# Performance work log

Hardware: AMD Instinct MI355X
Metric: run time of the kernel (lower is better)

Reference implementation:

```python
import jax, jax.numpy as jnp
import numpy as np

EPS = 1e-6
GAMMA = 1.0
NB_EXPERTS = 16
DEPTH = 4  # log2(NB_EXPERTS), complete binary tree
K = 4
ENTROPY_REG = 0.01


def smooth_step(t, gamma=GAMMA):
    # DSelect-k / COMET smooth-step: 0 below -gamma/2, 1 above gamma/2, cubic between
    poly = (-2.0 / gamma ** 3) * t ** 3 + (3.0 / (2.0 * gamma)) * t + 0.5
    return jnp.where(t <= -gamma / 2, 0.0, jnp.where(t >= gamma / 2, 1.0, poly))


def setup_inputs() -> dict:
    key = jax.random.key(0)
    k0, k1, k2, k3 = jax.random.split(key, 4)
    B, D_IN, D_OUT = 8192, 1024, 768
    # h: expert outputs, already stacked (torch code concatenates a list on dim 2)
    h = jax.random.normal(k0, (B, D_OUT, NB_EXPERTS), jnp.float32)
    x = jax.random.normal(k1, (B, D_IN), jnp.float32)
    # selector weights: uniform(-gamma/100, gamma/100), level-order over internal nodes
    sel_w = jax.random.uniform(k2, (NB_EXPERTS - 1, K, D_IN), jnp.float32, -GAMMA / 100, GAMMA / 100)
    # leaf output layers: uniform(-0.05, 0.05) weights, zero bias
    leaf_w = jax.random.uniform(k3, (NB_EXPERTS, K, D_IN), jnp.float32, -0.05, 0.05)
    leaf_b = jnp.zeros((NB_EXPERTS, K), jnp.float32)
    return {"h": h, "x": x, "sel_w": sel_w, "leaf_w": leaf_w, "leaf_b": leaf_b}


def reference(h, x, sel_w, leaf_w, leaf_b):
    B = x.shape[0]
    # gate activations at all internal nodes (level order): (B, E-1, K)
    gates = smooth_step(jnp.einsum('bd,nkd->bnk', x, sel_w))
    # expand root->leaf path products level by level; [left, right] interleave
    # matches the recursive concat order on dim 2 in the torch code
    probs = jnp.ones((B, 1, K), x.dtype)
    start = 0
    for d in range(DEPTH):
        n = 2 ** d
        g = gates[:, start:start + n, :]               # (B, n, K)
        probs = jnp.stack([probs * g, probs * (1.0 - g)], axis=2).reshape(B, 2 * n, K)
        start += n
    # probs: (B, E, K) leaf routing probabilities
    # leaf logits a_bij + log(prob)
    a = jnp.einsum('bd,ekd->bek', x, leaf_w) + leaf_b  # (B, E, K)
    logp = jnp.where(probs < 1e-5, -jnp.inf, jnp.log(probs + 1e-6))
    s = a + logp                                       # (B, E, K)
    # softmax over all k*E leaf slots (flatten order irrelevant to the sums below)
    w = jax.nn.softmax(s.reshape(B, -1), axis=-1).reshape(B, NB_EXPERTS, K)
    # permutation_mask is k stacked identities -> einsum is identity; sum over k
    w_expert = jnp.sum(w, axis=2)                      # (B, E)
    w_norm = w_expert / jnp.sum(w_expert, axis=-1, keepdims=True)
    # aggregate expert outputs
    y_agg = jnp.einsum('bde,be->bd', h, w_norm)        # (B, D_OUT)
    # sparsity statistics (keep torch shapes: w_permuted is (B,1,1,E))
    w4 = w_norm[:, None, None, :]
    s_concat = jnp.where(w4 < 1e-5, jnp.ones_like(w4), jnp.zeros_like(w4))
    soft_averages = jnp.mean(w4, axis=(0, 1, 2))       # (E,)
    hard_averages = jnp.mean(1.0 - s_concat, axis=(0, 1, 2))  # (E,)
    # entropy regularization, summed over leaves = sum over (E,K) per sample
    p = jnp.clip(probs, EPS, None)
    reg = ENTROPY_REG * jnp.mean(jnp.sum(-(p + EPS) * jnp.log(p + EPS), axis=(1, 2)))
    return (y_agg, soft_averages, hard_averages, s_concat, reg)
```

## Files before the change

kernel.cpp:

```cpp
#include <hip/hip_runtime.h>
#include <math.h>

#define NB 8192
#define DIN 1024
#define DOUT 768
#define NE 16

#define BM 128
#define BN 128
#define BK 32
#define KSPLIT 4
#define KCHUNK (DIN / KSPLIT)
#define NTILES (KCHUNK / BK)
#define LDT 36

#define NSEL 60
#define NCOL 124

#define Y_OFF    0
#define SOFT_OFF 6291456
#define HARD_OFF 6291472
#define SC_OFF   6291488
#define REG_OFF  6422560

__device__ __forceinline__ float smooth_step_f(float t) {
  float p = -2.0f * t * t * t + 1.5f * t + 0.5f;
  p = (t <= -0.5f) ? 0.0f : p;
  p = (t >= 0.5f) ? 1.0f : p;
  return p;
}

__global__ __launch_bounds__(256) void k1_gemm(
    const float* __restrict__ x, const float* __restrict__ sel_w,
    const float* __restrict__ leaf_w, float* __restrict__ Gp)
{
  __shared__ float xs[BM * LDT];
  __shared__ float wsm[BN * LDT];
  const int t  = threadIdx.x;
  const int b0 = blockIdx.x * BM;
  const int k0 = blockIdx.y * KCHUNK;
  const int rg = t >> 4;
  const int cg = t & 15;

  float acc[8][8];
#pragma unroll
  for (int i = 0; i < 8; ++i)
#pragma unroll
    for (int j = 0; j < 8; ++j) acc[i][j] = 0.0f;

  int fr[4], fk[4];
#pragma unroll
  for (int m = 0; m < 4; ++m) { int f = t + 256 * m; fr[m] = f >> 3; fk[m] = (f & 7) * 4; }

  float4 px[4], pw[4];
#pragma unroll
  for (int m = 0; m < 4; ++m) {
    int kb = k0 + fk[m];
    px[m] = *(const float4*)(x + (size_t)(b0 + fr[m]) * DIN + kb);
    int c = fr[m];
    if (c < NSEL)      pw[m] = *(const float4*)(sel_w + (size_t)c * DIN + kb);
    else if (c < NCOL) pw[m] = *(const float4*)(leaf_w + (size_t)(c - NSEL) * DIN + kb);
    else               pw[m] = make_float4(0.f, 0.f, 0.f, 0.f);
  }

  for (int kt = 0; kt < NTILES; ++kt) {
#pragma unroll
    for (int m = 0; m < 4; ++m) {
      *(float4*)(&xs[fr[m] * LDT + fk[m]])  = px[m];
      *(float4*)(&wsm[fr[m] * LDT + fk[m]]) = pw[m];
    }
    __syncthreads();
    if (kt + 1 < NTILES) {
      int kb0 = k0 + (kt + 1) * BK;
#pragma unroll
      for (int m = 0; m < 4; ++m) {
        int kb = kb0 + fk[m];
        px[m] = *(const float4*)(x + (size_t)(b0 + fr[m]) * DIN + kb);
        int c = fr[m];
        if (c < NSEL)      pw[m] = *(const float4*)(sel_w + (size_t)c * DIN + kb);
        else if (c < NCOL) pw[m] = *(const float4*)(leaf_w + (size_t)(c - NSEL) * DIN + kb);
        else               pw[m] = make_float4(0.f, 0.f, 0.f, 0.f);
      }
    }
#pragma unroll 4
    for (int kk = 0; kk < BK; ++kk) {
      float xv[8], wv[8];
#pragma unroll
      for (int i = 0; i < 8; ++i) xv[i] = xs[(rg + 16 * i) * LDT + kk];
#pragma unroll
      for (int j = 0; j < 8; ++j) wv[j] = wsm[(cg + 16 * j) * LDT + kk];
#pragma unroll
      for (int i = 0; i < 8; ++i)
#pragma unroll
        for (int j = 0; j < 8; ++j)
          acc[i][j] = fmaf(xv[i], wv[j], acc[i][j]);
    }
    __syncthreads();
  }

  const int ks = blockIdx.y;
#pragma unroll
  for (int i = 0; i < 8; ++i) {
    int gr = b0 + rg + 16 * i;
#pragma unroll
    for (int j = 0; j < 8; ++j) {
      int c = cg + 16 * j;
      Gp[((size_t)ks * NB + gr) * BN + c] = acc[i][j];
    }
  }
}

__global__ __launch_bounds__(256) void k2_rows(
    const float* __restrict__ Gp, const float* __restrict__ leaf_b,
    float* __restrict__ wnorm, float* __restrict__ out)
{
  const int b = blockIdx.x * 256 + threadIdx.x;
  const size_t rb = (size_t)b * BN;

  float s_arr[64];
  float rsum = 0.0f;

#pragma unroll
  for (int k = 0; k < 4; ++k) {
    float gt[15];
#pragma unroll
    for (int n = 0; n < 15; ++n) {
      float v = 0.0f;
#pragma unroll
      for (int s = 0; s < KSPLIT; ++s) v += Gp[(size_t)s * NB * BN + rb + n * 4 + k];
      gt[n] = smooth_step_f(v);
    }
#pragma unroll
    for (int l = 0; l < 16; ++l) {
      float g0 = gt[0];
      float g1 = gt[1 + (l >> 3)];
      float g2 = gt[3 + (l >> 2)];
      float g3 = gt[7 + (l >> 1)];
      float f0 = ((l >> 3) & 1) ? (1.0f - g0) : g0;
      float f1 = ((l >> 2) & 1) ? (1.0f - g1) : g1;
      float f2 = ((l >> 1) & 1) ? (1.0f - g2) : g2;
      float f3 = (l & 1)        ? (1.0f - g3) : g3;
      float p = ((f0 * f1) * f2) * f3;
      float pc = fmaxf(p, 1e-6f);
      float lg = logf(pc + 1e-6f);
      rsum += -(pc + 1e-6f) * lg;
      float av = 0.0f;
#pragma unroll
      for (int s = 0; s < KSPLIT; ++s) av += Gp[(size_t)s * NB * BN + rb + NSEL + l * 4 + k];
      av += leaf_b[l * 4 + k];
      s_arr[l * 4 + k] = (p < 1e-5f) ? -INFINITY : (av + lg);
    }
  }

  float m = s_arr[0];
#pragma unroll
  for (int i = 1; i < 64; ++i) m = fmaxf(m, s_arr[i]);

  float we[16];
#pragma unroll
  for (int e = 0; e < 16; ++e) we[e] = 0.0f;
  float sum = 0.0f;
#pragma unroll
  for (int e = 0; e < 16; ++e)
#pragma unroll
    for (int k = 0; k < 4; ++k) {
      float wv = expf(s_arr[e * 4 + k] - m);
      sum += wv;
      we[e] += wv;
    }
  float inv = 1.0f / sum;

  float softp[16], hardp[16];
#pragma unroll
  for (int e = 0; e < 16; ++e) {
    float wn = we[e] * inv;
    softp[e] = wn;
    float sc = (wn < 1e-5f) ? 1.0f : 0.0f;
    hardp[e] = 1.0f - sc;
    wnorm[(size_t)b * NE + e] = wn;
    out[SC_OFF + (size_t)b * NE + e] = sc;
  }

#pragma unroll
  for (int e = 0; e < 16; ++e) {
    float v = softp[e];
    v += __shfl_down(v, 32, 64); v += __shfl_down(v, 16, 64); v += __shfl_down(v, 8, 64);
    v += __shfl_down(v, 4, 64);  v += __shfl_down(v, 2, 64);  v += __shfl_down(v, 1, 64);
    if ((threadIdx.x & 63) == 0) atomicAdd(&out[SOFT_OFF + e], v * (1.0f / (float)NB));
    float hv = hardp[e];
    hv += __shfl_down(hv, 32, 64); hv += __shfl_down(hv, 16, 64); hv += __shfl_down(hv, 8, 64);
    hv += __shfl_down(hv, 4, 64);  hv += __shfl_down(hv, 2, 64);  hv += __shfl_down(hv, 1, 64);
    if ((threadIdx.x & 63) == 0) atomicAdd(&out[HARD_OFF + e], hv * (1.0f / (float)NB));
  }
  {
    float v = rsum;
    v += __shfl_down(v, 32, 64); v += __shfl_down(v, 16, 64); v += __shfl_down(v, 8, 64);
    v += __shfl_down(v, 4, 64);  v += __shfl_down(v, 2, 64);  v += __shfl_down(v, 1, 64);
    if ((threadIdx.x & 63) == 0) atomicAdd(&out[REG_OFF], v * (0.01f / (float)NB));
  }
}

__global__ __launch_bounds__(256) void k3_yagg(
    const float* __restrict__ h, const float* __restrict__ wnorm,
    float* __restrict__ out)
{
  const int b = blockIdx.x;
  __shared__ float wl[NE];
  if (threadIdx.x < NE) wl[threadIdx.x] = wnorm[(size_t)b * NE + threadIdx.x];
  __syncthreads();
  float w[NE];
#pragma unroll
  for (int e = 0; e < NE; ++e) w[e] = wl[e];

#pragma unroll
  for (int mm = 0; mm < 3; ++mm) {
    int d = threadIdx.x + 256 * mm;
    const float4* hp = (const float4*)(h + ((size_t)b * DOUT + d) * NE);
    float4 h0 = hp[0], h1 = hp[1], h2 = hp[2], h3 = hp[3];
    float acc;
    acc  = h0.x * w[0]  + h0.y * w[1]  + h0.z * w[2]  + h0.w * w[3];
    acc += h1.x * w[4]  + h1.y * w[5]  + h1.z * w[6]  + h1.w * w[7];
    acc += h2.x * w[8]  + h2.y * w[9]  + h2.z * w[10] + h2.w * w[11];
    acc += h3.x * w[12] + h3.y * w[13] + h3.z * w[14] + h3.w * w[15];
    out[(size_t)b * DOUT + d] = acc;
  }
}

extern "C" void kernel_launch(void* const* d_in, const int* in_sizes, int n_in,
                              void* d_out, int out_size, void* d_ws, size_t ws_size,
                              hipStream_t stream)
{
  const float* h      = (const float*)d_in[0];
  const float* x      = (const float*)d_in[1];
  const float* sel_w  = (const float*)d_in[2];
  const float* leaf_w = (const float*)d_in[3];
  const float* leaf_b = (const float*)d_in[4];
  float* out = (float*)d_out;

  float* wnorm = (float*)d_ws;
  float* Gp    = wnorm + (size_t)NB * NE;

  hipMemsetAsync(out + SOFT_OFF, 0, 32 * sizeof(float), stream);
  hipMemsetAsync(out + REG_OFF, 0, sizeof(float), stream);

  k1_gemm<<<dim3(NB / BM, KSPLIT), 256, 0, stream>>>(x, sel_w, leaf_w, Gp);
  k2_rows<<<NB / 256, 256, 0, stream>>>(Gp, leaf_b, wnorm, out);
  k3_yagg<<<NB, 256, 0, stream>>>(h, wnorm, out);
}
```

Measured before the change: 651.8 us.

## Fuse gate GEMM with per-row routing softmax, drop split-K partials

Merges the split-K GEMM kernel and the per-row routing kernel into one kernel. Each block computes a 32-row by 128-column tile over the full K dimension, stages the results in shared memory, and lets 32 threads run the gating, softmax and statistics. This removes the global round trip of four partial-sum buffers and one kernel launch. In exchange it reloads the full weight matrix for every 32 rows and leaves 224 of 256 threads idle during the serial per-row phase.

```diff
diff --git a/kernel.cpp b/kernel.cpp
--- a/kernel.cpp
+++ b/kernel.cpp
@@ -6,18 +6,14 @@
 #define DOUT 768
 #define NE 16
 
-#define BM 128
-#define BN 128
-#define BK 32
-#define KSPLIT 4
-#define KCHUNK (DIN / KSPLIT)
-#define NTILES (KCHUNK / BK)
-#define LDT 36
-
+#define RB 32
+#define KT 64
+#define NT (DIN / KT)
+#define LDW 68
+#define LDG 129
 #define NSEL 60
 #define NCOL 124
 
-#define Y_OFF    0
 #define SOFT_OFF 6291456
 #define HARD_OFF 6291472
 #define SC_OFF   6291488
@@ -30,173 +26,168 @@
   return p;
 }
 
-__global__ __launch_bounds__(256) void k1_gemm(
+__global__ __launch_bounds__(256) void k12_gate(
     const float* __restrict__ x, const float* __restrict__ sel_w,
-    const float* __restrict__ leaf_w, float* __restrict__ Gp)
-{
-  __shared__ float xs[BM * LDT];
-  __shared__ float wsm[BN * LDT];
-  const int t  = threadIdx.x;
-  const int b0 = blockIdx.x * BM;
-  const int k0 = blockIdx.y * KCHUNK;
-  const int rg = t >> 4;
-  const int cg = t & 15;
-
-  float acc[8][8];
-#pragma unroll
-  for (int i = 0; i < 8; ++i)
-#pragma unroll
-    for (int j = 0; j < 8; ++j) acc[i][j] = 0.0f;
-
-  int fr[4], fk[4];
-#pragma unroll
-  for (int m = 0; m < 4; ++m) { int f = t + 256 * m; fr[m] = f >> 3; fk[m] = (f & 7) * 4; }
-
-  float4 px[4], pw[4];
-#pragma unroll
-  for (int m = 0; m < 4; ++m) {
-    int kb = k0 + fk[m];
-    px[m] = *(const float4*)(x + (size_t)(b0 + fr[m]) * DIN + kb);
-    int c = fr[m];
-    if (c < NSEL)      pw[m] = *(const float4*)(sel_w + (size_t)c * DIN + kb);
-    else if (c < NCOL) pw[m] = *(const float4*)(leaf_w + (size_t)(c - NSEL) * DIN + kb);
-    else               pw[m] = make_float4(0.f, 0.f, 0.f, 0.f);
-  }
-
-  for (int kt = 0; kt < NTILES; ++kt) {
-#pragma unroll
-    for (int m = 0; m < 4; ++m) {
-      *(float4*)(&xs[fr[m] * LDT + fk[m]])  = px[m];
-      *(float4*)(&wsm[fr[m] * LDT + fk[m]]) = pw[m];
-    }
-    __syncthreads();
-    if (kt + 1 < NTILES) {
-      int kb0 = k0 + (kt + 1) * BK;
-#pragma unroll
-      for (int m = 0; m < 4; ++m) {
-        int kb = kb0 + fk[m];
-        px[m] = *(const float4*)(x + (size_t)(b0 + fr[m]) * DIN + kb);
-        int c = fr[m];
-        if (c < NSEL)      pw[m] = *(const float4*)(sel_w + (size_t)c * DIN + kb);
-        else if (c < NCOL) pw[m] = *(const float4*)(leaf_w + (size_t)(c - NSEL) * DIN + kb);
-        else               pw[m] = make_float4(0.f, 0.f, 0.f, 0.f);
-      }
-    }
-#pragma unroll 4
-    for (int kk = 0; kk < BK; ++kk) {
-      float xv[8], wv[8];
-#pragma unroll
-      for (int i = 0; i < 8; ++i) xv[i] = xs[(rg + 16 * i) * LDT + kk];
-#pragma unroll
-      for (int j = 0; j < 8; ++j) wv[j] = wsm[(cg + 16 * j) * LDT + kk];
-#pragma unroll
-      for (int i = 0; i < 8; ++i)
-#pragma unroll
-        for (int j = 0; j < 8; ++j)
-          acc[i][j] = fmaf(xv[i], wv[j], acc[i][j]);
-    }
-    __syncthreads();
-  }
-
-  const int ks = blockIdx.y;
-#pragma unroll
-  for (int i = 0; i < 8; ++i) {
-    int gr = b0 + rg + 16 * i;
-#pragma unroll
-    for (int j = 0; j < 8; ++j) {
-      int c = cg + 16 * j;
-      Gp[((size_t)ks * NB + gr) * BN + c] = acc[i][j];
-    }
-  }
-}
-
-__global__ __launch_bounds__(256) void k2_rows(
-    const float* __restrict__ Gp, const float* __restrict__ leaf_b,
+    const float* __restrict__ leaf_w, const float* __restrict__ leaf_b,
     float* __restrict__ wnorm, float* __restrict__ out)
 {
-  const int b = blockIdx.x * 256 + threadIdx.x;
-  const size_t rb = (size_t)b * BN;
-
-  float s_arr[64];
-  float rsum = 0.0f;
-
-#pragma unroll
-  for (int k = 0; k < 4; ++k) {
-    float gt[15];
-#pragma unroll
-    for (int n = 0; n < 15; ++n) {
-      float v = 0.0f;
-#pragma unroll
-      for (int s = 0; s < KSPLIT; ++s) v += Gp[(size_t)s * NB * BN + rb + n * 4 + k];
-      gt[n] = smooth_step_f(v);
-    }
-#pragma unroll
-    for (int l = 0; l < 16; ++l) {
-      float g0 = gt[0];
-      float g1 = gt[1 + (l >> 3)];
-      float g2 = gt[3 + (l >> 2)];
-      float g3 = gt[7 + (l >> 1)];
-      float f0 = ((l >> 3) & 1) ? (1.0f - g0) : g0;
-      float f1 = ((l >> 2) & 1) ? (1.0f - g1) : g1;
-      float f2 = ((l >> 1) & 1) ? (1.0f - g2) : g2;
-      float f3 = (l & 1)        ? (1.0f - g3) : g3;
-      float p = ((f0 * f1) * f2) * f3;
-      float pc = fmaxf(p, 1e-6f);
-      float lg = logf(pc + 1e-6f);
-      rsum += -(pc + 1e-6f) * lg;
-      float av = 0.0f;
-#pragma unroll
-      for (int s = 0; s < KSPLIT; ++s) av += Gp[(size_t)s * NB * BN + rb + NSEL + l * 4 + k];
-      av += leaf_b[l * 4 + k];
-      s_arr[l * 4 + k] = (p < 1e-5f) ? -INFINITY : (av + lg);
-    }
-  }
-
-  float m = s_arr[0];
-#pragma unroll
-  for (int i = 1; i < 64; ++i) m = fmaxf(m, s_arr[i]);
-
-  float we[16];
-#pragma unroll
-  for (int e = 0; e < 16; ++e) we[e] = 0.0f;
-  float sum = 0.0f;
-#pragma unroll
-  for (int e = 0; e < 16; ++e)
+  __shared__ float xs[RB * LDW];
+  __shared__ float wsm[128 * LDW];
+  __shared__ float gsm[RB * LDG];
+  const int t  = threadIdx.x;
+  const int b0 = blockIdx.x * RB;
+  const int tr = t >> 5;
+  const int tc = t & 31;
+
+  float acc[4][4];
+#pragma unroll
+  for (int i = 0; i < 4; ++i)
+#pragma unroll
+    for (int j = 0; j < 4; ++j) acc[i][j] = 0.0f;
+
+  int xr[2], xk[2];
+#pragma unroll
+  for (int m = 0; m < 2; ++m) { int f = t + 256 * m; xr[m] = f >> 4; xk[m] = (f & 15) * 4; }
+  int wc[8], wk[8];
+#pragma unroll
+  for (int m = 0; m < 8; ++m) { int f = t + 256 * m; wc[m] = f >> 4; wk[m] = (f & 15) * 4; }
+
+  float4 px[2], pw[8];
+#pragma unroll
+  for (int m = 0; m < 2; ++m)
+    px[m] = *(const float4*)(x + (size_t)(b0 + xr[m]) * DIN + xk[m]);
+#pragma unroll
+  for (int m = 0; m < 8; ++m) {
+    int c = wc[m];
+    if (c < NSEL)      pw[m] = *(const float4*)(sel_w + (size_t)c * DIN + wk[m]);
+    else if (c < NCOL) pw[m] = *(const float4*)(leaf_w + (size_t)(c - NSEL) * DIN + wk[m]);
+    else               pw[m] = make_float4(0.f, 0.f, 0.f, 0.f);
+  }
+
+  for (int kt = 0; kt < NT; ++kt) {
+#pragma unroll
+    for (int m = 0; m < 2; ++m) *(float4*)(&xs[xr[m] * LDW + xk[m]]) = px[m];
+#pragma unroll
+    for (int m = 0; m < 8; ++m) *(float4*)(&wsm[wc[m] * LDW + wk[m]]) = pw[m];
+    __syncthreads();
+    if (kt + 1 < NT) {
+      int kb = (kt + 1) * KT;
+#pragma unroll
+      for (int m = 0; m < 2; ++m)
+        px[m] = *(const float4*)(x + (size_t)(b0 + xr[m]) * DIN + kb + xk[m]);
+#pragma unroll
+      for (int m = 0; m < 8; ++m) {
+        int c = wc[m];
+        if (c < NSEL)      pw[m] = *(const float4*)(sel_w + (size_t)c * DIN + kb + wk[m]);
+        else if (c < NCOL) pw[m] = *(const float4*)(leaf_w + (size_t)(c - NSEL) * DIN + kb + wk[m]);
+        else               pw[m] = make_float4(0.f, 0.f, 0.f, 0.f);
+      }
+    }
+#pragma unroll 8
+    for (int kk = 0; kk < KT; kk += 4) {
+      float4 xv[4], wv[4];
+#pragma unroll
+      for (int i = 0; i < 4; ++i) xv[i] = *(const float4*)(&xs[(tr + 8 * i) * LDW + kk]);
+#pragma unroll
+      for (int j = 0; j < 4; ++j) wv[j] = *(const float4*)(&wsm[(tc + 32 * j) * LDW + kk]);
+#pragma unroll
+      for (int i = 0; i < 4; ++i)
+#pragma unroll
+        for (int j = 0; j < 4; ++j) {
+          acc[i][j] = fmaf(xv[i].x, wv[j].x, acc[i][j]);
+          acc[i][j] = fmaf(xv[i].y, wv[j].y, acc[i][j]);
+          acc[i][j] = fmaf(xv[i].z, wv[j].z, acc[i][j]);
+          acc[i][j] = fmaf(xv[i].w, wv[j].w, acc[i][j]);
+        }
+    }
+    __syncthreads();
+  }
+
+#pragma unroll
+  for (int i = 0; i < 4; ++i)
+#pragma unroll
+    for (int j = 0; j < 4; ++j)
+      gsm[(tr + 8 * i) * LDG + tc + 32 * j] = acc[i][j];
+  __syncthreads();
+
+  if (t < RB) {
+    const int b = b0 + t;
+    const float* gr = &gsm[t * LDG];
+
+    float s_arr[64];
+    float rsum = 0.0f;
 #pragma unroll
     for (int k = 0; k < 4; ++k) {
-      float wv = expf(s_arr[e * 4 + k] - m);
-      sum += wv;
-      we[e] += wv;
-    }
-  float inv = 1.0f / sum;
-
-  float softp[16], hardp[16];
-#pragma unroll
-  for (int e = 0; e < 16; ++e) {
-    float wn = we[e] * inv;
-    softp[e] = wn;
-    float sc = (wn < 1e-5f) ? 1.0f : 0.0f;
-    hardp[e] = 1.0f - sc;
-    wnorm[(size_t)b * NE + e] = wn;
-    out[SC_OFF + (size_t)b * NE + e] = sc;
-  }
-
-#pragma unroll
-  for (int e = 0; e < 16; ++e) {
-    float v = softp[e];
-    v += __shfl_down(v, 32, 64); v += __shfl_down(v, 16, 64); v += __shfl_down(v, 8, 64);
-    v += __shfl_down(v, 4, 64);  v += __shfl_down(v, 2, 64);  v += __shfl_down(v, 1, 64);
-    if ((threadIdx.x & 63) == 0) atomicAdd(&out[SOFT_OFF + e], v * (1.0f / (float)NB));
-    float hv = hardp[e];
-    hv += __shfl_down(hv, 32, 64); hv += __shfl_down(hv, 16, 64); hv += __shfl_down(hv, 8, 64);
-    hv += __shfl_down(hv, 4, 64);  hv += __shfl_down(hv, 2, 64);  hv += __shfl_down(hv, 1, 64);
-    if ((threadIdx.x & 63) == 0) atomicAdd(&out[HARD_OFF + e], hv * (1.0f / (float)NB));
-  }
-  {
-    float v = rsum;
-    v += __shfl_down(v, 32, 64); v += __shfl_down(v, 16, 64); v += __shfl_down(v, 8, 64);
-    v += __shfl_down(v, 4, 64);  v += __shfl_down(v, 2, 64);  v += __shfl_down(v, 1, 64);
-    if ((threadIdx.x & 63) == 0) atomicAdd(&out[REG_OFF], v * (0.01f / (float)NB));
+      float gt[15];
+#pragma unroll
+      for (int n = 0; n < 15; ++n) gt[n] = smooth_step_f(gr[n * 4 + k]);
+#pragma unroll
+      for (int l = 0; l < 16; ++l) {
+        float g0 = gt[0];
+        float g1 = gt[1 + (l >> 3)];
+        float g2 = gt[3 + (l >> 2)];
+        float g3 = gt[7 + (l >> 1)];
+        float f0 = ((l >> 3) & 1) ? (1.0f - g0) : g0;
+        float f1 = ((l >> 2) & 1) ? (1.0f - g1) : g1;
+        float f2 = ((l >> 1) & 1) ? (1.0f - g2) : g2;
+        float f3 = (l & 1)        ? (1.0f - g3) : g3;
+        float p = ((f0 * f1) * f2) * f3;
+        float pc = fmaxf(p, 1e-6f);
+        float lg = logf(pc + 1e-6f);
+        rsum += -(pc + 1e-6f) * lg;
+        float av = gr[NSEL + l * 4 + k] + leaf_b[l * 4 + k];
+        s_arr[l * 4 + k] = (p < 1e-5f) ? -INFINITY : (av + lg);
+      }
+    }
+
+    float m = s_arr[0];
+#pragma unroll
+    for (int i = 1; i < 64; ++i) m = fmaxf(m, s_arr[i]);
+
+    float we[16];
+#pragma unroll
+    for (int e = 0; e < 16; ++e) we[e] = 0.0f;
+    float sum = 0.0f;
+#pragma unroll
+    for (int e = 0; e < 16; ++e)
+#pragma unroll
+      for (int k = 0; k < 4; ++k) {
+        float wv = expf(s_arr[e * 4 + k] - m);
+        sum += wv;
+        we[e] += wv;
+      }
+    float inv = 1.0f / sum;
+
+    float softp[16], hardp[16];
+#pragma unroll
+    for (int e = 0; e < 16; ++e) {
+      float wn = we[e] * inv;
+      softp[e] = wn;
+      float sc = (wn < 1e-5f) ? 1.0f : 0.0f;
+      hardp[e] = 1.0f - sc;
+      wnorm[(size_t)b * NE + e] = wn;
+      out[SC_OFF + (size_t)b * NE + e] = sc;
+    }
+
+#pragma unroll
+    for (int e = 0; e < 16; ++e) {
+      float v = softp[e];
+      v += __shfl_down(v, 16, 64); v += __shfl_down(v, 8, 64);
+      v += __shfl_down(v, 4, 64);  v += __shfl_down(v, 2, 64); v += __shfl_down(v, 1, 64);
+      float hv = hardp[e];
+      hv += __shfl_down(hv, 16, 64); hv += __shfl_down(hv, 8, 64);
+      hv += __shfl_down(hv, 4, 64);  hv += __shfl_down(hv, 2, 64); hv += __shfl_down(hv, 1, 64);
+      if (t == 0) {
+        atomicAdd(&out[SOFT_OFF + e], v * (1.0f / (float)NB));
+        atomicAdd(&out[HARD_OFF + e], hv * (1.0f / (float)NB));
+      }
+    }
+    {
+      float v = rsum;
+      v += __shfl_down(v, 16, 64); v += __shfl_down(v, 8, 64);
+      v += __shfl_down(v, 4, 64);  v += __shfl_down(v, 2, 64); v += __shfl_down(v, 1, 64);
+      if (t == 0) atomicAdd(&out[REG_OFF], v * (0.01f / (float)NB));
+    }
   }
 }
 
@@ -238,12 +229,10 @@
   float* out = (float*)d_out;
 
   float* wnorm = (float*)d_ws;
-  float* Gp    = wnorm + (size_t)NB * NE;
 
   hipMemsetAsync(out + SOFT_OFF, 0, 32 * sizeof(float), stream);
   hipMemsetAsync(out + REG_OFF, 0, sizeof(float), stream);
 
-  k1_gemm<<<dim3(NB / BM, KSPLIT), 256, 0, stream>>>(x, sel_w, leaf_w, Gp);
-  k2_rows<<<NB / 256, 256, 0, stream>>>(Gp, leaf_b, wnorm, out);
+  k12_gate<<<NB / RB, 256, 0, stream>>>(x, sel_w, leaf_w, leaf_b, wnorm, out);
   k3_yagg<<<NB, 256, 0, stream>>>(h, wnorm, out);
 }
```

New measurement: 659.7 us. About the same (+1.2%).
